# Performance work log

Measured on AMD Instinct MI355X. Metric: run time of the kernel, lower is better.

## Reference

```python
import jax, jax.numpy as jnp
import numpy as np

COMMITMENT_COST = 0.25


def setup_inputs() -> dict:
    key = jax.random.key(0)
    k1, k2 = jax.random.split(key)
    B, C, L, H, W = 4, 64, 16, 32, 32
    K = 1024
    inputs = jax.random.normal(k1, (B, C, L, H, W), dtype=jnp.float32)
    # matches torch init: uniform_(-1/K, 1/K)
    codebook = jax.random.uniform(k2, (K, C), dtype=jnp.float32,
                                  minval=-1.0 / K, maxval=1.0 / K)
    return {"inputs": inputs, "codebook": codebook}


def reference(inputs, codebook):
    B, C, L, H, W = inputs.shape
    # [B,C,L,H,W] -> [N, D] with D == embedding_dim == C
    x = jnp.transpose(inputs, (0, 2, 3, 4, 1)).reshape(-1, C).astype(jnp.float32)
    cb = codebook.astype(jnp.float32)
    # squared euclidean distances (argmin identical to p=2 cdist argmin)
    d2 = (jnp.sum(x * x, axis=1, keepdims=True)
          - 2.0 * (x @ cb.T)
          + jnp.sum(cb * cb, axis=1))  # [N, K]
    encoding_indices = jnp.argmin(d2, axis=1)  # [N]
    # one-hot @ codebook == direct gather
    quantized = cb[encoding_indices].astype(inputs.dtype)  # [N, D]
    quantized = jnp.transpose(quantized.reshape(B, L, H, W, C), (0, 4, 1, 2, 3))
    e_latent_loss = jnp.mean((jax.lax.stop_gradient(quantized) - inputs) ** 2)
    q_latent_loss = jnp.mean((quantized - jax.lax.stop_gradient(inputs)) ** 2)
    loss = q_latent_loss + COMMITMENT_COST * e_latent_loss
    # straight-through estimator
    quantized_st = inputs + jax.lax.stop_gradient(quantized - inputs)
    return quantized_st, loss, encoding_indices[:, None]
```

## Files before the change

kernel.cpp:

```cpp
#include <hip/hip_runtime.h>

constexpr int Cc   = 64;
constexpr int Kc   = 1024;
constexpr int Dc   = 64;
constexpr int LHWc = 16 * 32 * 32;
constexpr int Nc   = 4 * LHWc;
constexpr int QSIZE    = 4 * Cc * LHWc;
constexpr int OFF_LOSS = QSIZE;
constexpr int OFF_IDX  = QSIZE + 1;

constexpr int BLK_ROWS = 256;
constexpr int XPAD     = 68;

typedef __attribute__((ext_vector_type(8))) short short8;
typedef __attribute__((ext_vector_type(4))) float f32x4;

static __device__ __forceinline__ unsigned short f2bf(float f) {
    unsigned u = __float_as_uint(f);
    u += 0x7FFFu + ((u >> 16) & 1u);
    return (unsigned short)(u >> 16);
}
static __device__ __forceinline__ float bf2f(unsigned short h) {
    return __uint_as_float(((unsigned)h) << 16);
}

__global__ __launch_bounds__(256) void vq_prep(
    const float* __restrict__ cb, float* __restrict__ out,
    unsigned short* __restrict__ cbh, unsigned short* __restrict__ cbl,
    float* __restrict__ c2)
{
    const int t  = threadIdx.x;
    const int k0 = blockIdx.x * 64;
    if (blockIdx.x == 0 && t == 0) out[OFF_LOSS] = 0.0f;

    const int d  = t & 63;
#pragma unroll
    for (int r = 0; r < 16; ++r) {
        const int k = k0 + r * 4 + (t >> 6);
        const float v = cb[(size_t)k * Dc + d];
        unsigned short h = f2bf(v);
        cbh[(size_t)k * Dc + d] = h;
        cbl[(size_t)k * Dc + d] = f2bf(v - bf2f(h));
    }
    if (t < 64) {
        const int k = k0 + t;
        const float* c = cb + (size_t)k * Dc;
        float s = 0.f;
#pragma unroll
        for (int dd = 0; dd < Dc; ++dd) s = __builtin_fmaf(c[dd], c[dd], s);
        c2[k] = s;
    }
}

__global__ __launch_bounds__(512, 2) void vq_main(
    const float* __restrict__ in, const float* __restrict__ codebook,
    const unsigned short* __restrict__ cbh,
    const unsigned short* __restrict__ cbl,
    const float* __restrict__ c2g, float* __restrict__ out)
{
    __shared__ float  xs[BLK_ROWS][XPAD];
    __shared__ float  xs2[BLK_ROWS];
    __shared__ short8 xfh[2048];
    __shared__ short8 xfl[2048];
    __shared__ float  candV1[8][BLK_ROWS];
    __shared__ float  candV2[8][BLK_ROWS];
    __shared__ unsigned candKs[8][BLK_ROWS];
    __shared__ int    kws[BLK_ROWS];

    const int tid  = threadIdx.x;
    const int lane = tid & 63;
    const int w    = __builtin_amdgcn_readfirstlane(tid >> 6);
    const int col  = lane & 15;
    const int g    = lane >> 4;

    const int bq = blockIdx.x >> 6;
    const int p0 = (blockIdx.x & 63) * BLK_ROWS;
    const size_t inBase = (size_t)bq * (Cc * LHWc) + p0;

#pragma unroll
    for (int i = 0; i < 32; ++i) {
        int idx = i * 512 + tid;
        int d = idx >> 8, row = idx & 255;
        xs[row][d] = in[inBase + (size_t)d * LHWc + row];
    }
    __syncthreads();

    if (tid < BLK_ROWS) {
        float s = 0.f;
#pragma unroll
        for (int d = 0; d < Dc; ++d) s = __builtin_fmaf(xs[tid][d], xs[tid][d], s);
        xs2[tid] = s;
    }

#pragma unroll
    for (int j = 0; j < 4; ++j) {
        const int c  = tid + j * 512;
        const int t  = c >> 7;
        const int kt = (c >> 6) & 1;
        const int l  = c & 63;
        const int row = t * 16 + (l & 15);
        const int d0  = kt * 32 + (l >> 4) * 8;
        f32x4 v0 = *(const f32x4*)&xs[row][d0];
        f32x4 v1 = *(const f32x4*)&xs[row][d0 + 4];
        short8 h8, l8;
#pragma unroll
        for (int e = 0; e < 4; ++e) {
            unsigned short ha = f2bf(v0[e]);
            h8[e]     = (short)ha;
            l8[e]     = (short)f2bf(v0[e] - bf2f(ha));
            unsigned short hb = f2bf(v1[e]);
            h8[4 + e] = (short)hb;
            l8[4 + e] = (short)f2bf(v1[e] - bf2f(hb));
        }
        xfh[c] = h8; xfl[c] = l8;
    }
    __syncthreads();

    short8 Ah[8][2], Al[8][2];
    const size_t cbase = (size_t)(w * 128 + col) * Dc + g * 8;
#pragma unroll
    for (int ct = 0; ct < 8; ++ct) {
#pragma unroll
        for (int kt = 0; kt < 2; ++kt) {
            Ah[ct][kt] = *(const short8*)(cbh + cbase + ct * 16 * Dc + kt * 32);
            Al[ct][kt] = *(const short8*)(cbl + cbase + ct * 16 * Dc + kt * 32);
        }
    }
    float c2r[8][4];
#pragma unroll
    for (int ct = 0; ct < 8; ++ct)
#pragma unroll
        for (int r = 0; r < 4; ++r)
            c2r[ct][r] = c2g[w * 128 + ct * 16 + g * 4 + r];
    const int kbl = w * 128 + g * 4;

#pragma unroll 1
    for (int t = 0; t < 16; ++t) {
        const short8 xh0 = xfh[t * 128 + lane];
        const short8 xh1 = xfh[t * 128 + 64 + lane];
        const short8 xl0 = xfl[t * 128 + lane];
        const short8 xl1 = xfl[t * 128 + 64 + lane];
        const float  x2l = xs2[t * 16 + col];

        float bV = 3.4e38f, sV = 3.4e38f;
        int   bK = 0, sK = 0;

#pragma unroll
        for (int ct = 0; ct < 8; ++ct) {
            f32x4 acc = {0.f, 0.f, 0.f, 0.f};
            acc = __builtin_amdgcn_mfma_f32_16x16x32_bf16(Ah[ct][0], xh0, acc, 0, 0, 0);
            acc = __builtin_amdgcn_mfma_f32_16x16x32_bf16(Ah[ct][1], xh1, acc, 0, 0, 0);
            acc = __builtin_amdgcn_mfma_f32_16x16x32_bf16(Ah[ct][0], xl0, acc, 0, 0, 0);
            acc = __builtin_amdgcn_mfma_f32_16x16x32_bf16(Ah[ct][1], xl1, acc, 0, 0, 0);
            acc = __builtin_amdgcn_mfma_f32_16x16x32_bf16(Al[ct][0], xh0, acc, 0, 0, 0);
            acc = __builtin_amdgcn_mfma_f32_16x16x32_bf16(Al[ct][1], xh1, acc, 0, 0, 0);
#pragma unroll
            for (int r = 0; r < 4; ++r) {
                float d2 = __builtin_fmaf(-2.f, acc[r], x2l);
                float v  = d2 + c2r[ct][r];
                int   k  = kbl + ct * 16 + r;
                bool  c1 = v < bV;
                float nb  = c1 ? v : bV;
                int   nbk = c1 ? k : bK;
                float mx  = c1 ? bV : v;
                int   mxk = c1 ? bK : k;
                bool  c2_ = mx < sV;
                sV = c2_ ? mx : sV;
                sK = c2_ ? mxk : sK;
                bV = nb; bK = nbk;
            }
        }

#pragma unroll
        for (int m = 16; m <= 32; m <<= 1) {
            float ob  = __shfl_xor(bV, m, 64);
            int   obk = __shfl_xor(bK, m, 64);
            float os  = __shfl_xor(sV, m, 64);
            int   osk = __shfl_xor(sK, m, 64);
            bool  c1 = ob < bV;
            float nb  = c1 ? ob : bV;
            int   nbk = c1 ? obk : bK;
            float mx  = c1 ? bV : ob;
            int   mxk = c1 ? bK : obk;
            bool  c3 = os < sV;
            float ms  = c3 ? os : sV;
            int   msk = c3 ? osk : sK;
            bool  c4 = mx < ms;
            sV = c4 ? mx : ms;
            sK = c4 ? mxk : msk;
            bV = nb; bK = nbk;
        }
        if (g == 0) {
            const int row = t * 16 + col;
            candV1[w][row] = bV;
            candV2[w][row] = sV;
            candKs[w][row] = (unsigned)bK | ((unsigned)sK << 16);
        }
    }
    __syncthreads();

    if (tid < BLK_ROWS) {
        const int row = tid;
        unsigned long long b = ~0ull, s = ~0ull;
#pragma unroll
        for (int wv = 0; wv < 8; ++wv) {
            unsigned ks = candKs[wv][row];
            unsigned long long p1 =
                ((unsigned long long)__float_as_uint(candV1[wv][row]) << 32) | (ks & 0xFFFFu);
            unsigned long long p2 =
                ((unsigned long long)__float_as_uint(candV2[wv][row]) << 32) | (ks >> 16);
            unsigned long long nb = p1 < b ? p1 : b;
            unsigned long long mx = p1 < b ? b : p1;
            s = mx < s ? mx : s; b = nb;
            nb = p2 < b ? p2 : b;
            mx = p2 < b ? b : p2;
            s = mx < s ? mx : s; b = nb;
        }
        kws[row] = (int)((b & 0x3FFu) | ((s & 0x3FFu) << 16));
    }
    __syncthreads();

    {
        const int row = tid >> 1;
        const int ci  = tid & 1;
        const int pr  = kws[row];
        const int k   = ci ? ((pr >> 16) & 0x3FF) : (pr & 0x3FF);
        const float* cbr = codebook + (size_t)k * Dc;
        float a0 = 0.f, a1 = 0.f, a2 = 0.f, a3 = 0.f;
#pragma unroll
        for (int d16 = 0; d16 < 4; ++d16) {
            f32x4 cv0 = *(const f32x4*)(cbr + d16 * 16);
            f32x4 cv1 = *(const f32x4*)(cbr + d16 * 16 + 4);
            f32x4 cv2 = *(const f32x4*)(cbr + d16 * 16 + 8);
            f32x4 cv3 = *(const f32x4*)(cbr + d16 * 16 + 12);
            const float* xr = &xs[row][d16 * 16];
#pragma unroll
            for (int e = 0; e < 4; ++e) {
                a0 = __builtin_fmaf(xr[e],      cv0[e], a0);
                a1 = __builtin_fmaf(xr[4 + e],  cv1[e], a1);
                a2 = __builtin_fmaf(xr[8 + e],  cv2[e], a2);
                a3 = __builtin_fmaf(xr[12 + e], cv3[e], a3);
            }
        }
        float a  = (a0 + a1) + (a2 + a3);
        float d2 = __builtin_fmaf(-2.f, a, xs2[row]) + c2g[k];
        unsigned long long pk =
            ((unsigned long long)__float_as_uint(d2) << 32) | (unsigned)k;
        unsigned long long o = __shfl_xor(pk, 1, 64);
        pk = o < pk ? o : pk;
        if (ci == 0) {
            const int kwin = (int)(pk & 0x3FFu);
            kws[row] = kwin;
            out[OFF_IDX + (size_t)blockIdx.x * BLK_ROWS + row] = (float)kwin;
        }
    }
    __syncthreads();

    {
        const int row = tid & 255;
        const int cp  = tid >> 8;
        const int kw  = kws[row];
        const float* cbw = codebook + (size_t)kw * Dc + cp * 32;
        float* qout = out + inBase + row;
        float ls = 0.f;
#pragma unroll
        for (int j = 0; j < 32; ++j) {
            const int c = cp * 32 + j;
            float qv = cbw[j];
            qout[(size_t)c * LHWc] = qv;
            float e = qv - xs[row][c];
            ls = __builtin_fmaf(e, e, ls);
        }
#pragma unroll
        for (int off = 32; off > 0; off >>= 1) ls += __shfl_down(ls, off, 64);
        if (lane == 0) atomicAdd(&out[OFF_LOSS], ls * (1.25f / (float)QSIZE));
    }
}

extern "C" void kernel_launch(void* const* d_in, const int* in_sizes, int n_in,
                              void* d_out, int out_size, void* d_ws, size_t ws_size,
                              hipStream_t stream) {
    const float* in = (const float*)d_in[0];
    const float* cb = (const float*)d_in[1];
    float* out = (float*)d_out;
    (void)in_sizes; (void)n_in; (void)out_size; (void)ws_size;

    unsigned short* cbh = (unsigned short*)d_ws;
    unsigned short* cbl = cbh + (size_t)Kc * Dc;
    float*          c2  = (float*)(cbl + (size_t)Kc * Dc);

    vq_prep<<<dim3(16), dim3(256), 0, stream>>>(cb, out, cbh, cbl, c2);
    vq_main<<<dim3(Nc / BLK_ROWS), dim3(512), 0, stream>>>(in, cb, cbh, cbl, c2, out);
}
```

Baseline: 139.3 us.

## Restructure VQ kernel to 128-row blocks with 16 waves and no fp32 smem tile

Halves rows per block and doubles waves to 16 per 1024-thread block, so each wave holds 64 codebook entries in registers instead of 128. The fp32 input tile in shared memory is dropped: inputs are read from global memory straight into the bf16 hi/lo fragments, with partial squared norms computed on the fly. The per-row x² term is left out of the argmin scan, and a +0.25 offset is folded into c2. The exact rescoring and loss stages re-read inputs from global memory, and the candidate merge is split across two threads per row. The aim is lower register and LDS pressure and better occupancy, at the cost of extra global re-reads of the inputs.

```diff
diff --git a/kernel.cpp b/kernel.cpp
--- a/kernel.cpp
+++ b/kernel.cpp
@@ -9,8 +9,8 @@
 constexpr int OFF_LOSS = QSIZE;
 constexpr int OFF_IDX  = QSIZE + 1;
 
-constexpr int BLK_ROWS = 256;
-constexpr int XPAD     = 68;
+constexpr int BLK_ROWS = 128;
+constexpr int WAVES    = 16;
 
 typedef __attribute__((ext_vector_type(8))) short short8;
 typedef __attribute__((ext_vector_type(4))) float f32x4;
@@ -52,20 +52,20 @@
     }
 }
 
-__global__ __launch_bounds__(512, 2) void vq_main(
+__global__ __launch_bounds__(1024) void vq_main(
     const float* __restrict__ in, const float* __restrict__ codebook,
     const unsigned short* __restrict__ cbh,
     const unsigned short* __restrict__ cbl,
     const float* __restrict__ c2g, float* __restrict__ out)
 {
-    __shared__ float  xs[BLK_ROWS][XPAD];
-    __shared__ float  xs2[BLK_ROWS];
-    __shared__ short8 xfh[2048];
-    __shared__ short8 xfl[2048];
-    __shared__ float  candV1[8][BLK_ROWS];
-    __shared__ float  candV2[8][BLK_ROWS];
-    __shared__ unsigned candKs[8][BLK_ROWS];
-    __shared__ int    kws[BLK_ROWS];
+    __shared__ short8   xfh[1024];
+    __shared__ short8   xfl[1024];
+    __shared__ float    xpart[BLK_ROWS][8];
+    __shared__ float    xs2[BLK_ROWS];
+    __shared__ float    cV1[WAVES][BLK_ROWS];
+    __shared__ float    cV2[WAVES][BLK_ROWS];
+    __shared__ unsigned cK [WAVES][BLK_ROWS];
+    __shared__ unsigned kpack[BLK_ROWS];
 
     const int tid  = threadIdx.x;
     const int lane = tid & 63;
@@ -73,80 +73,67 @@
     const int col  = lane & 15;
     const int g    = lane >> 4;
 
-    const int bq = blockIdx.x >> 6;
-    const int p0 = (blockIdx.x & 63) * BLK_ROWS;
+    const int bq = blockIdx.x >> 7;
+    const int p0 = (blockIdx.x & 127) * BLK_ROWS;
     const size_t inBase = (size_t)bq * (Cc * LHWc) + p0;
 
-#pragma unroll
-    for (int i = 0; i < 32; ++i) {
-        int idx = i * 512 + tid;
-        int d = idx >> 8, row = idx & 255;
-        xs[row][d] = in[inBase + (size_t)d * LHWc + row];
-    }
-    __syncthreads();
-
-    if (tid < BLK_ROWS) {
-        float s = 0.f;
-#pragma unroll
-        for (int d = 0; d < Dc; ++d) s = __builtin_fmaf(xs[tid][d], xs[tid][d], s);
-        xs2[tid] = s;
-    }
-
-#pragma unroll
-    for (int j = 0; j < 4; ++j) {
-        const int c  = tid + j * 512;
+    short8 Ah[4][2], Al[4][2];
+    float  c2r[4][4];
+#pragma unroll
+    for (int ct = 0; ct < 4; ++ct) {
+        const size_t cb0 = (size_t)(w * 64 + ct * 16 + col) * Dc + g * 8;
+#pragma unroll
+        for (int kt = 0; kt < 2; ++kt) {
+            Ah[ct][kt] = *(const short8*)(cbh + cb0 + kt * 32);
+            Al[ct][kt] = *(const short8*)(cbl + cb0 + kt * 32);
+        }
+#pragma unroll
+        for (int r = 0; r < 4; ++r)
+            c2r[ct][r] = c2g[w * 64 + ct * 16 + g * 4 + r] + 0.25f;
+    }
+
+    {
+        const int c  = tid;
         const int t  = c >> 7;
         const int kt = (c >> 6) & 1;
-        const int l  = c & 63;
-        const int row = t * 16 + (l & 15);
-        const int d0  = kt * 32 + (l >> 4) * 8;
-        f32x4 v0 = *(const f32x4*)&xs[row][d0];
-        f32x4 v1 = *(const f32x4*)&xs[row][d0 + 4];
+        const int gi = (c >> 4) & 3;
+        const int cl = c & 15;
+        const int row = t * 16 + cl;
+        const float* xp = in + inBase + (size_t)(kt * 32 + gi * 8) * LHWc + row;
+        float v[8];
+#pragma unroll
+        for (int j = 0; j < 8; ++j) v[j] = xp[(size_t)j * LHWc];
+        float p = 0.f;
+#pragma unroll
+        for (int j = 0; j < 8; ++j) p = __builtin_fmaf(v[j], v[j], p);
         short8 h8, l8;
 #pragma unroll
-        for (int e = 0; e < 4; ++e) {
-            unsigned short ha = f2bf(v0[e]);
-            h8[e]     = (short)ha;
-            l8[e]     = (short)f2bf(v0[e] - bf2f(ha));
-            unsigned short hb = f2bf(v1[e]);
-            h8[4 + e] = (short)hb;
-            l8[4 + e] = (short)f2bf(v1[e] - bf2f(hb));
+        for (int j = 0; j < 8; ++j) {
+            unsigned short hv = f2bf(v[j]);
+            h8[j] = (short)hv;
+            l8[j] = (short)f2bf(v[j] - bf2f(hv));
         }
         xfh[c] = h8; xfl[c] = l8;
-    }
-    __syncthreads();
-
-    short8 Ah[8][2], Al[8][2];
-    const size_t cbase = (size_t)(w * 128 + col) * Dc + g * 8;
-#pragma unroll
-    for (int ct = 0; ct < 8; ++ct) {
-#pragma unroll
-        for (int kt = 0; kt < 2; ++kt) {
-            Ah[ct][kt] = *(const short8*)(cbh + cbase + ct * 16 * Dc + kt * 32);
-            Al[ct][kt] = *(const short8*)(cbl + cbase + ct * 16 * Dc + kt * 32);
-        }
-    }
-    float c2r[8][4];
-#pragma unroll
-    for (int ct = 0; ct < 8; ++ct)
-#pragma unroll
-        for (int r = 0; r < 4; ++r)
-            c2r[ct][r] = c2g[w * 128 + ct * 16 + g * 4 + r];
-    const int kbl = w * 128 + g * 4;
+        xpart[row][kt * 4 + gi] = p;
+    }
+    __syncthreads();
+    if (tid < BLK_ROWS) {
+        const float* q = xpart[tid];
+        xs2[tid] = ((q[0] + q[1]) + (q[2] + q[3])) + ((q[4] + q[5]) + (q[6] + q[7]));
+    }
 
 #pragma unroll 1
-    for (int t = 0; t < 16; ++t) {
+    for (int t = 0; t < 8; ++t) {
         const short8 xh0 = xfh[t * 128 + lane];
         const short8 xh1 = xfh[t * 128 + 64 + lane];
         const short8 xl0 = xfl[t * 128 + lane];
         const short8 xl1 = xfl[t * 128 + 64 + lane];
-        const float  x2l = xs2[t * 16 + col];
 
         float bV = 3.4e38f, sV = 3.4e38f;
         int   bK = 0, sK = 0;
 
 #pragma unroll
-        for (int ct = 0; ct < 8; ++ct) {
+        for (int ct = 0; ct < 4; ++ct) {
             f32x4 acc = {0.f, 0.f, 0.f, 0.f};
             acc = __builtin_amdgcn_mfma_f32_16x16x32_bf16(Ah[ct][0], xh0, acc, 0, 0, 0);
             acc = __builtin_amdgcn_mfma_f32_16x16x32_bf16(Ah[ct][1], xh1, acc, 0, 0, 0);
@@ -156,13 +143,12 @@
             acc = __builtin_amdgcn_mfma_f32_16x16x32_bf16(Al[ct][1], xh1, acc, 0, 0, 0);
 #pragma unroll
             for (int r = 0; r < 4; ++r) {
-                float d2 = __builtin_fmaf(-2.f, acc[r], x2l);
-                float v  = d2 + c2r[ct][r];
-                int   k  = kbl + ct * 16 + r;
-                bool  c1 = v < bV;
-                float nb  = c1 ? v : bV;
+                float vv = __builtin_fmaf(-2.f, acc[r], c2r[ct][r]);
+                const int k = w * 64 + ct * 16 + g * 4 + r;
+                bool  c1 = vv < bV;
+                float nb  = c1 ? vv : bV;
                 int   nbk = c1 ? k : bK;
-                float mx  = c1 ? bV : v;
+                float mx  = c1 ? bV : vv;
                 int   mxk = c1 ? bK : k;
                 bool  c2_ = mx < sV;
                 sV = c2_ ? mx : sV;
@@ -192,55 +178,73 @@
         }
         if (g == 0) {
             const int row = t * 16 + col;
-            candV1[w][row] = bV;
-            candV2[w][row] = sV;
-            candKs[w][row] = (unsigned)bK | ((unsigned)sK << 16);
-        }
-    }
-    __syncthreads();
-
-    if (tid < BLK_ROWS) {
-        const int row = tid;
-        unsigned long long b = ~0ull, s = ~0ull;
+            cV1[w][row] = bV;
+            cV2[w][row] = sV;
+            cK [w][row] = (unsigned)bK | ((unsigned)sK << 16);
+        }
+    }
+    __syncthreads();
+
+    if (tid < 2 * BLK_ROWS) {
+        const int row = tid >> 1;
+        const int h   = tid & 1;
+        float b = 3.4e38f, s = 3.4e38f;
+        int   bk = 0, sk = 0;
 #pragma unroll
         for (int wv = 0; wv < 8; ++wv) {
-            unsigned ks = candKs[wv][row];
-            unsigned long long p1 =
-                ((unsigned long long)__float_as_uint(candV1[wv][row]) << 32) | (ks & 0xFFFFu);
-            unsigned long long p2 =
-                ((unsigned long long)__float_as_uint(candV2[wv][row]) << 32) | (ks >> 16);
-            unsigned long long nb = p1 < b ? p1 : b;
-            unsigned long long mx = p1 < b ? b : p1;
-            s = mx < s ? mx : s; b = nb;
-            nb = p2 < b ? p2 : b;
-            mx = p2 < b ? b : p2;
-            s = mx < s ? mx : s; b = nb;
-        }
-        kws[row] = (int)((b & 0x3FFu) | ((s & 0x3FFu) << 16));
-    }
-    __syncthreads();
-
-    {
+            const int wj = h * 8 + wv;
+            const unsigned ks = cK[wj][row];
+            const float v1 = cV1[wj][row];
+            const float v2 = cV2[wj][row];
+            const int  k1 = (int)(ks & 0xFFFFu);
+            const int  k2 = (int)(ks >> 16);
+            {
+                bool c1 = v1 < b;
+                float mx = c1 ? b : v1;  int mxk = c1 ? bk : k1;
+                b  = c1 ? v1 : b;        bk  = c1 ? k1 : bk;
+                bool c2_ = mx < s;  s = c2_ ? mx : s;  sk = c2_ ? mxk : sk;
+            }
+            {
+                bool c1 = v2 < b;
+                float mx = c1 ? b : v2;  int mxk = c1 ? bk : k2;
+                b  = c1 ? v2 : b;        bk  = c1 ? k2 : bk;
+                bool c2_ = mx < s;  s = c2_ ? mx : s;  sk = c2_ ? mxk : sk;
+            }
+        }
+        float ob  = __shfl_xor(b, 1, 64);
+        int   obk = __shfl_xor(bk, 1, 64);
+        float os  = __shfl_xor(s, 1, 64);
+        int   osk = __shfl_xor(sk, 1, 64);
+        if (h == 0) {
+            bool  c1 = ob < b;
+            float nb  = c1 ? ob : b;
+            int   nbk = c1 ? obk : bk;
+            float mx  = c1 ? b : ob;
+            int   mxk = c1 ? bk : obk;
+            bool  c3 = os < s;
+            float ms  = c3 ? os : s;
+            int   msk = c3 ? osk : sk;
+            bool  c4 = mx < ms;
+            int   fsk = c4 ? mxk : msk;
+            kpack[row] = (unsigned)nbk | ((unsigned)fsk << 16);
+        }
+    }
+    __syncthreads();
+
+    if (tid < 2 * BLK_ROWS) {
         const int row = tid >> 1;
         const int ci  = tid & 1;
-        const int pr  = kws[row];
-        const int k   = ci ? ((pr >> 16) & 0x3FF) : (pr & 0x3FF);
+        const unsigned pr = kpack[row];
+        const int k = ci ? (int)(pr >> 16) : (int)(pr & 0xFFFFu);
         const float* cbr = codebook + (size_t)k * Dc;
+        const float* xr  = in + inBase + row;
         float a0 = 0.f, a1 = 0.f, a2 = 0.f, a3 = 0.f;
 #pragma unroll
-        for (int d16 = 0; d16 < 4; ++d16) {
-            f32x4 cv0 = *(const f32x4*)(cbr + d16 * 16);
-            f32x4 cv1 = *(const f32x4*)(cbr + d16 * 16 + 4);
-            f32x4 cv2 = *(const f32x4*)(cbr + d16 * 16 + 8);
-            f32x4 cv3 = *(const f32x4*)(cbr + d16 * 16 + 12);
-            const float* xr = &xs[row][d16 * 16];
-#pragma unroll
-            for (int e = 0; e < 4; ++e) {
-                a0 = __builtin_fmaf(xr[e],      cv0[e], a0);
-                a1 = __builtin_fmaf(xr[4 + e],  cv1[e], a1);
-                a2 = __builtin_fmaf(xr[8 + e],  cv2[e], a2);
-                a3 = __builtin_fmaf(xr[12 + e], cv3[e], a3);
-            }
+        for (int d = 0; d < 64; d += 4) {
+            a0 = __builtin_fmaf(xr[(size_t)(d + 0) * LHWc], cbr[d + 0], a0);
+            a1 = __builtin_fmaf(xr[(size_t)(d + 1) * LHWc], cbr[d + 1], a1);
+            a2 = __builtin_fmaf(xr[(size_t)(d + 2) * LHWc], cbr[d + 2], a2);
+            a3 = __builtin_fmaf(xr[(size_t)(d + 3) * LHWc], cbr[d + 3], a3);
         }
         float a  = (a0 + a1) + (a2 + a3);
         float d2 = __builtin_fmaf(-2.f, a, xs2[row]) + c2g[k];
@@ -250,25 +254,26 @@
         pk = o < pk ? o : pk;
         if (ci == 0) {
             const int kwin = (int)(pk & 0x3FFu);
-            kws[row] = kwin;
+            kpack[row] = (unsigned)kwin;
             out[OFF_IDX + (size_t)blockIdx.x * BLK_ROWS + row] = (float)kwin;
         }
     }
     __syncthreads();
 
     {
-        const int row = tid & 255;
-        const int cp  = tid >> 8;
-        const int kw  = kws[row];
-        const float* cbw = codebook + (size_t)kw * Dc + cp * 32;
+        const int row = tid & 127;
+        const int cp  = tid >> 7;
+        const int kw  = (int)kpack[row];
+        const float* cbw = codebook + (size_t)kw * Dc + cp * 8;
+        const float* xr  = in + inBase + row;
         float* qout = out + inBase + row;
         float ls = 0.f;
 #pragma unroll
-        for (int j = 0; j < 32; ++j) {
-            const int c = cp * 32 + j;
+        for (int j = 0; j < 8; ++j) {
+            const int c = cp * 8 + j;
             float qv = cbw[j];
             qout[(size_t)c * LHWc] = qv;
-            float e = qv - xs[row][c];
+            float e = qv - xr[(size_t)c * LHWc];
             ls = __builtin_fmaf(e, e, ls);
         }
 #pragma unroll
@@ -290,5 +295,5 @@
     float*          c2  = (float*)(cbl + (size_t)Kc * Dc);
 
     vq_prep<<<dim3(16), dim3(256), 0, stream>>>(cb, out, cbh, cbl, c2);
-    vq_main<<<dim3(Nc / BLK_ROWS), dim3(512), 0, stream>>>(in, cb, cbh, cbl, c2, out);
-}
+    vq_main<<<dim3(Nc / BLK_ROWS), dim3(1024), 0, stream>>>(in, cb, cbh, cbl, c2, out);
+}
```

Measured after the change: 202.6 us. 45.4% more time.

## Fold codebook prep into main kernel and seed MFMA accumulators with -c2/2

Applied to the files above, without the earlier changes.

Removes the separate prep kernel, so each block now computes codebook squared norms into shared memory and converts the codebook to bf16 hi/lo fragments in registers directly from fp32. The distance expression is rewritten as a max over dot minus half the norm, by seeding the MFMA accumulator with -0.5*c2. This drops the per-element x2 add and -2 scaling, and the top-2 tracking becomes a per-register fmax chain. The cross-wave candidate merge is split over all 512 threads, and the x tile padding changes to 65. The cost is that every block redundantly reads the full codebook and recomputes its norms, which adds global traffic and prologue work per block.

```diff
diff --git a/kernel.cpp b/kernel.cpp
--- a/kernel.cpp
+++ b/kernel.cpp
@@ -10,7 +10,8 @@
 constexpr int OFF_IDX  = QSIZE + 1;
 
 constexpr int BLK_ROWS = 256;
-constexpr int XPAD     = 68;
+constexpr int NW       = 8;
+constexpr int XPAD     = 65;
 
 typedef __attribute__((ext_vector_type(8))) short short8;
 typedef __attribute__((ext_vector_type(4))) float f32x4;
@@ -24,48 +25,24 @@
     return __uint_as_float(((unsigned)h) << 16);
 }
 
-__global__ __launch_bounds__(256) void vq_prep(
-    const float* __restrict__ cb, float* __restrict__ out,
-    unsigned short* __restrict__ cbh, unsigned short* __restrict__ cbl,
-    float* __restrict__ c2)
+__global__ void vq_zero(float* __restrict__ out) {
+    out[OFF_LOSS] = 0.0f;
+}
+
+__global__ __launch_bounds__(512)
+__attribute__((amdgpu_waves_per_eu(2, 2))) void vq_main(
+    const float* __restrict__ in, const float* __restrict__ codebook,
+    float* __restrict__ out)
 {
-    const int t  = threadIdx.x;
-    const int k0 = blockIdx.x * 64;
-    if (blockIdx.x == 0 && t == 0) out[OFF_LOSS] = 0.0f;
-
-    const int d  = t & 63;
-#pragma unroll
-    for (int r = 0; r < 16; ++r) {
-        const int k = k0 + r * 4 + (t >> 6);
-        const float v = cb[(size_t)k * Dc + d];
-        unsigned short h = f2bf(v);
-        cbh[(size_t)k * Dc + d] = h;
-        cbl[(size_t)k * Dc + d] = f2bf(v - bf2f(h));
-    }
-    if (t < 64) {
-        const int k = k0 + t;
-        const float* c = cb + (size_t)k * Dc;
-        float s = 0.f;
-#pragma unroll
-        for (int dd = 0; dd < Dc; ++dd) s = __builtin_fmaf(c[dd], c[dd], s);
-        c2[k] = s;
-    }
-}
-
-__global__ __launch_bounds__(512, 2) void vq_main(
-    const float* __restrict__ in, const float* __restrict__ codebook,
-    const unsigned short* __restrict__ cbh,
-    const unsigned short* __restrict__ cbl,
-    const float* __restrict__ c2g, float* __restrict__ out)
-{
-    __shared__ float  xs[BLK_ROWS][XPAD];
-    __shared__ float  xs2[BLK_ROWS];
-    __shared__ short8 xfh[2048];
-    __shared__ short8 xfl[2048];
-    __shared__ float  candV1[8][BLK_ROWS];
-    __shared__ float  candV2[8][BLK_ROWS];
-    __shared__ unsigned candKs[8][BLK_ROWS];
-    __shared__ int    kws[BLK_ROWS];
+    __shared__ float    xs[BLK_ROWS][XPAD];
+    __shared__ short8   xfh[2048];
+    __shared__ short8   xfl[2048];
+    __shared__ float    c2s[Kc];
+    __shared__ float    xs2[BLK_ROWS];
+    __shared__ float    cV1[NW][BLK_ROWS];
+    __shared__ float    cV2[NW][BLK_ROWS];
+    __shared__ unsigned cK [NW][BLK_ROWS];
+    __shared__ unsigned kws[BLK_ROWS];
 
     const int tid  = threadIdx.x;
     const int lane = tid & 63;
@@ -82,6 +59,38 @@
         int idx = i * 512 + tid;
         int d = idx >> 8, row = idx & 255;
         xs[row][d] = in[inBase + (size_t)d * LHWc + row];
+    }
+
+#pragma unroll
+    for (int j = 0; j < 2; ++j) {
+        const int k = tid + j * 512;
+        const float* c = codebook + (size_t)k * Dc;
+        float s = 0.f;
+#pragma unroll
+        for (int d = 0; d < Dc; ++d) s = __builtin_fmaf(c[d], c[d], s);
+        c2s[k] = s;
+    }
+
+    short8 Ah[8][2], Al[8][2];
+#pragma unroll
+    for (int ct = 0; ct < 8; ++ct) {
+        const float* cr = codebook + (size_t)(w * 128 + ct * 16 + col) * Dc + g * 8;
+#pragma unroll
+        for (int kt = 0; kt < 2; ++kt) {
+            f32x4 v0 = *(const f32x4*)(cr + kt * 32);
+            f32x4 v1 = *(const f32x4*)(cr + kt * 32 + 4);
+            short8 h8, l8;
+#pragma unroll
+            for (int e = 0; e < 4; ++e) {
+                unsigned short ha = f2bf(v0[e]);
+                h8[e]     = (short)ha;
+                l8[e]     = (short)f2bf(v0[e] - bf2f(ha));
+                unsigned short hb = f2bf(v1[e]);
+                h8[4 + e] = (short)hb;
+                l8[4 + e] = (short)f2bf(v1[e] - bf2f(hb));
+            }
+            Ah[ct][kt] = h8; Al[ct][kt] = l8;
+        }
     }
     __syncthreads();
 
@@ -114,25 +123,17 @@
         }
         xfh[c] = h8; xfl[c] = l8;
     }
-    __syncthreads();
-
-    short8 Ah[8][2], Al[8][2];
-    const size_t cbase = (size_t)(w * 128 + col) * Dc + g * 8;
+
+    f32x4 seed[8];
 #pragma unroll
     for (int ct = 0; ct < 8; ++ct) {
-#pragma unroll
-        for (int kt = 0; kt < 2; ++kt) {
-            Ah[ct][kt] = *(const short8*)(cbh + cbase + ct * 16 * Dc + kt * 32);
-            Al[ct][kt] = *(const short8*)(cbl + cbase + ct * 16 * Dc + kt * 32);
-        }
-    }
-    float c2r[8][4];
-#pragma unroll
-    for (int ct = 0; ct < 8; ++ct)
-#pragma unroll
-        for (int r = 0; r < 4; ++r)
-            c2r[ct][r] = c2g[w * 128 + ct * 16 + g * 4 + r];
-    const int kbl = w * 128 + g * 4;
+        f32x4 cv = *(const f32x4*)&c2s[w * 128 + ct * 16 + g * 4];
+#pragma unroll
+        for (int e = 0; e < 4; ++e) seed[ct][e] = -0.5f * (cv[e] + 0.25f);
+    }
+    __syncthreads();
+
+    const int kb = w * 128 + g * 4;
 
 #pragma unroll 1
     for (int t = 0; t < 16; ++t) {
@@ -140,14 +141,17 @@
         const short8 xh1 = xfh[t * 128 + 64 + lane];
         const short8 xl0 = xfl[t * 128 + lane];
         const short8 xl1 = xfl[t * 128 + 64 + lane];
-        const float  x2l = xs2[t * 16 + col];
-
-        float bV = 3.4e38f, sV = 3.4e38f;
-        int   bK = 0, sK = 0;
+
+        float bV[4], sV[4];
+        int   bK[4], sK[4];
+#pragma unroll
+        for (int r = 0; r < 4; ++r) {
+            bV[r] = -3.4e38f; sV[r] = -3.4e38f; bK[r] = 0; sK[r] = 0;
+        }
 
 #pragma unroll
         for (int ct = 0; ct < 8; ++ct) {
-            f32x4 acc = {0.f, 0.f, 0.f, 0.f};
+            f32x4 acc = seed[ct];
             acc = __builtin_amdgcn_mfma_f32_16x16x32_bf16(Ah[ct][0], xh0, acc, 0, 0, 0);
             acc = __builtin_amdgcn_mfma_f32_16x16x32_bf16(Ah[ct][1], xh1, acc, 0, 0, 0);
             acc = __builtin_amdgcn_mfma_f32_16x16x32_bf16(Ah[ct][0], xl0, acc, 0, 0, 0);
@@ -156,84 +160,124 @@
             acc = __builtin_amdgcn_mfma_f32_16x16x32_bf16(Al[ct][1], xh1, acc, 0, 0, 0);
 #pragma unroll
             for (int r = 0; r < 4; ++r) {
-                float d2 = __builtin_fmaf(-2.f, acc[r], x2l);
-                float v  = d2 + c2r[ct][r];
-                int   k  = kbl + ct * 16 + r;
-                bool  c1 = v < bV;
-                float nb  = c1 ? v : bV;
-                int   nbk = c1 ? k : bK;
-                float mx  = c1 ? bV : v;
-                int   mxk = c1 ? bK : k;
-                bool  c2_ = mx < sV;
-                sV = c2_ ? mx : sV;
-                sK = c2_ ? mxk : sK;
-                bV = nb; bK = nbk;
-            }
+                const float a  = acc[r];
+                const int   k  = kb + ct * 16 + r;
+                const float mn = fminf(a, bV[r]);
+                const bool  c1 = a > bV[r];
+                const int  mnk = c1 ? bK[r] : k;
+                bV[r] = fmaxf(a, bV[r]);
+                bK[r] = c1 ? k : bK[r];
+                const bool c2_ = mn > sV[r];
+                sV[r] = fmaxf(mn, sV[r]);
+                sK[r] = c2_ ? mnk : sK[r];
+            }
+        }
+
+        float b = bV[0], s = sV[0];
+        int   bk = bK[0], sk = sK[0];
+#pragma unroll
+        for (int r = 1; r < 4; ++r) {
+            const bool  c1 = bV[r] > b;
+            const float nb  = c1 ? bV[r] : b;
+            const int   nbk = c1 ? bK[r] : bk;
+            const float mn  = c1 ? b : bV[r];
+            const int   mnk = c1 ? bk : bK[r];
+            const float so  = c1 ? sV[r] : s;
+            const int   sok = c1 ? sK[r] : sk;
+            const bool  c2_ = so > mn;
+            s  = c2_ ? so : mn;
+            sk = c2_ ? sok : mnk;
+            b = nb; bk = nbk;
         }
 
 #pragma unroll
         for (int m = 16; m <= 32; m <<= 1) {
-            float ob  = __shfl_xor(bV, m, 64);
-            int   obk = __shfl_xor(bK, m, 64);
-            float os  = __shfl_xor(sV, m, 64);
-            int   osk = __shfl_xor(sK, m, 64);
-            bool  c1 = ob < bV;
-            float nb  = c1 ? ob : bV;
-            int   nbk = c1 ? obk : bK;
-            float mx  = c1 ? bV : ob;
-            int   mxk = c1 ? bK : obk;
-            bool  c3 = os < sV;
-            float ms  = c3 ? os : sV;
-            int   msk = c3 ? osk : sK;
-            bool  c4 = mx < ms;
-            sV = c4 ? mx : ms;
-            sK = c4 ? mxk : msk;
-            bV = nb; bK = nbk;
+            const float ob  = __shfl_xor(b, m, 64);
+            const int   obk = __shfl_xor(bk, m, 64);
+            const float os  = __shfl_xor(s, m, 64);
+            const int   osk = __shfl_xor(sk, m, 64);
+            const bool  c1 = ob > b;
+            const float nb  = c1 ? ob : b;
+            const int   nbk = c1 ? obk : bk;
+            const float mn  = c1 ? b : ob;
+            const int   mnk = c1 ? bk : obk;
+            const bool  c3 = os > s;
+            const float ms  = c3 ? os : s;
+            const int   msk = c3 ? osk : sk;
+            const bool  c4 = mn > ms;
+            s  = c4 ? mn : ms;
+            sk = c4 ? mnk : msk;
+            b = nb; bk = nbk;
         }
         if (g == 0) {
             const int row = t * 16 + col;
-            candV1[w][row] = bV;
-            candV2[w][row] = sV;
-            candKs[w][row] = (unsigned)bK | ((unsigned)sK << 16);
-        }
-    }
-    __syncthreads();
-
-    if (tid < BLK_ROWS) {
-        const int row = tid;
-        unsigned long long b = ~0ull, s = ~0ull;
-#pragma unroll
-        for (int wv = 0; wv < 8; ++wv) {
-            unsigned ks = candKs[wv][row];
-            unsigned long long p1 =
-                ((unsigned long long)__float_as_uint(candV1[wv][row]) << 32) | (ks & 0xFFFFu);
-            unsigned long long p2 =
-                ((unsigned long long)__float_as_uint(candV2[wv][row]) << 32) | (ks >> 16);
-            unsigned long long nb = p1 < b ? p1 : b;
-            unsigned long long mx = p1 < b ? b : p1;
-            s = mx < s ? mx : s; b = nb;
-            nb = p2 < b ? p2 : b;
-            mx = p2 < b ? b : p2;
-            s = mx < s ? mx : s; b = nb;
-        }
-        kws[row] = (int)((b & 0x3FFu) | ((s & 0x3FFu) << 16));
+            cV1[w][row] = b;
+            cV2[w][row] = s;
+            cK [w][row] = (unsigned)bk | ((unsigned)sk << 16);
+        }
+    }
+    __syncthreads();
+
+    {
+        const int row = tid >> 1;
+        const int h   = tid & 1;
+        float b = -3.4e38f, s = -3.4e38f;
+        int   bk = 0, sk = 0;
+#pragma unroll
+        for (int wv = 0; wv < 4; ++wv) {
+            const int wj = h * 4 + wv;
+            const unsigned ks = cK[wj][row];
+            const float v1 = cV1[wj][row];
+            const float v2 = cV2[wj][row];
+            const int  k1 = (int)(ks & 0xFFFFu);
+            const int  k2 = (int)(ks >> 16);
+            {
+                const bool c1 = v1 > b;
+                const float mn = c1 ? b : v1;  const int mnk = c1 ? bk : k1;
+                b  = c1 ? v1 : b;              bk  = c1 ? k1 : bk;
+                const bool c2_ = mn > s;  s = c2_ ? mn : s;  sk = c2_ ? mnk : sk;
+            }
+            {
+                const bool c1 = v2 > b;
+                const float mn = c1 ? b : v2;  const int mnk = c1 ? bk : k2;
+                b  = c1 ? v2 : b;              bk  = c1 ? k2 : bk;
+                const bool c2_ = mn > s;  s = c2_ ? mn : s;  sk = c2_ ? mnk : sk;
+            }
+        }
+        const float ob  = __shfl_xor(b, 1, 64);
+        const int   obk = __shfl_xor(bk, 1, 64);
+        const float os  = __shfl_xor(s, 1, 64);
+        const int   osk = __shfl_xor(sk, 1, 64);
+        if (h == 0) {
+            const bool  c1 = ob > b;
+            const float nb  = c1 ? ob : b;
+            const int   nbk = c1 ? obk : bk;
+            const float mn  = c1 ? b : ob;
+            const int   mnk = c1 ? bk : obk;
+            const bool  c3 = os > s;
+            const float ms  = c3 ? os : s;
+            const int   msk = c3 ? osk : sk;
+            const bool  c4 = mn > ms;
+            const int   fsk = c4 ? mnk : msk;
+            kws[row] = (unsigned)nbk | ((unsigned)fsk << 16);
+        }
     }
     __syncthreads();
 
     {
         const int row = tid >> 1;
         const int ci  = tid & 1;
-        const int pr  = kws[row];
-        const int k   = ci ? ((pr >> 16) & 0x3FF) : (pr & 0x3FF);
+        const unsigned pr = kws[row];
+        const int k = ci ? (int)(pr >> 16) : (int)(pr & 0xFFFFu);
         const float* cbr = codebook + (size_t)k * Dc;
         float a0 = 0.f, a1 = 0.f, a2 = 0.f, a3 = 0.f;
 #pragma unroll
-        for (int d16 = 0; d16 < 4; ++d16) {
-            f32x4 cv0 = *(const f32x4*)(cbr + d16 * 16);
-            f32x4 cv1 = *(const f32x4*)(cbr + d16 * 16 + 4);
-            f32x4 cv2 = *(const f32x4*)(cbr + d16 * 16 + 8);
-            f32x4 cv3 = *(const f32x4*)(cbr + d16 * 16 + 12);
-            const float* xr = &xs[row][d16 * 16];
+        for (int d4 = 0; d4 < 4; ++d4) {
+            f32x4 cv0 = *(const f32x4*)(cbr + d4 * 16);
+            f32x4 cv1 = *(const f32x4*)(cbr + d4 * 16 + 4);
+            f32x4 cv2 = *(const f32x4*)(cbr + d4 * 16 + 8);
+            f32x4 cv3 = *(const f32x4*)(cbr + d4 * 16 + 12);
+            const float* xr = &xs[row][d4 * 16];
 #pragma unroll
             for (int e = 0; e < 4; ++e) {
                 a0 = __builtin_fmaf(xr[e],      cv0[e], a0);
@@ -242,15 +286,15 @@
                 a3 = __builtin_fmaf(xr[12 + e], cv3[e], a3);
             }
         }
-        float a  = (a0 + a1) + (a2 + a3);
-        float d2 = __builtin_fmaf(-2.f, a, xs2[row]) + c2g[k];
+        const float a  = (a0 + a1) + (a2 + a3);
+        const float d2 = __builtin_fmaf(-2.f, a, xs2[row]) + c2s[k];
         unsigned long long pk =
             ((unsigned long long)__float_as_uint(d2) << 32) | (unsigned)k;
-        unsigned long long o = __shfl_xor(pk, 1, 64);
+        const unsigned long long o = __shfl_xor(pk, 1, 64);
         pk = o < pk ? o : pk;
         if (ci == 0) {
             const int kwin = (int)(pk & 0x3FFu);
-            kws[row] = kwin;
+            kws[row] = (unsigned)kwin;
             out[OFF_IDX + (size_t)blockIdx.x * BLK_ROWS + row] = (float)kwin;
         }
     }
@@ -259,7 +303,7 @@
     {
         const int row = tid & 255;
         const int cp  = tid >> 8;
-        const int kw  = kws[row];
+        const int kw  = (int)kws[row];
         const float* cbw = codebook + (size_t)kw * Dc + cp * 32;
         float* qout = out + inBase + row;
         float ls = 0.f;
@@ -283,12 +327,8 @@
     const float* in = (const float*)d_in[0];
     const float* cb = (const float*)d_in[1];
     float* out = (float*)d_out;
-    (void)in_sizes; (void)n_in; (void)out_size; (void)ws_size;
-
-    unsigned short* cbh = (unsigned short*)d_ws;
-    unsigned short* cbl = cbh + (size_t)Kc * Dc;
-    float*          c2  = (float*)(cbl + (size_t)Kc * Dc);
-
-    vq_prep<<<dim3(16), dim3(256), 0, stream>>>(cb, out, cbh, cbl, c2);
-    vq_main<<<dim3(Nc / BLK_ROWS), dim3(512), 0, stream>>>(in, cb, cbh, cbl, c2, out);
-}
+    (void)in_sizes; (void)n_in; (void)out_size; (void)d_ws; (void)ws_size;
+
+    vq_zero<<<dim3(1), dim3(1), 0, stream>>>(out);
+    vq_main<<<dim3(Nc / BLK_ROWS), dim3(512), 0, stream>>>(in, cb, out);
+}
```

Measured after the change: 164.9 us. 1.18x slower.

## Fold codebook norms into MFMA accumulator init and rescore all wave candidates exactly

Applied to the files above, without the earlier changes.

The argmin becomes an argmax of x·c − 0.5·|c|², because |x|² is constant per row. The precomputed −0.5·|c|² is loaded from shared memory as the initial MFMA accumulator, which removes the per-element FMA/add and the 32 registers that held codebook norms in the hot loop. The cross-wave top-2 merge by approximate values is dropped. Instead each row's 16 candidate indices (top-2 from each of 8 waves) are rescored in exact fp32, split across two threads. This adds codebook gathers and a 64-float register array in the refinement phase in exchange for less VALU work in the main loop.

```diff
diff --git a/kernel.cpp b/kernel.cpp
--- a/kernel.cpp
+++ b/kernel.cpp
@@ -10,6 +10,7 @@
 constexpr int OFF_IDX  = QSIZE + 1;
 
 constexpr int BLK_ROWS = 256;
+constexpr int NW       = 8;
 constexpr int XPAD     = 68;
 
 typedef __attribute__((ext_vector_type(8))) short short8;
@@ -27,7 +28,7 @@
 __global__ __launch_bounds__(256) void vq_prep(
     const float* __restrict__ cb, float* __restrict__ out,
     unsigned short* __restrict__ cbh, unsigned short* __restrict__ cbl,
-    float* __restrict__ c2)
+    float* __restrict__ c2, float* __restrict__ c2n)
 {
     const int t  = threadIdx.x;
     const int k0 = blockIdx.x * 64;
@@ -48,7 +49,8 @@
         float s = 0.f;
 #pragma unroll
         for (int dd = 0; dd < Dc; ++dd) s = __builtin_fmaf(c[dd], c[dd], s);
-        c2[k] = s;
+        c2[k]  = s;
+        c2n[k] = -0.5f * (s + 0.25f);
     }
 }
 
@@ -56,16 +58,16 @@
     const float* __restrict__ in, const float* __restrict__ codebook,
     const unsigned short* __restrict__ cbh,
     const unsigned short* __restrict__ cbl,
-    const float* __restrict__ c2g, float* __restrict__ out)
+    const float* __restrict__ c2g, const float* __restrict__ c2ng,
+    float* __restrict__ out)
 {
-    __shared__ float  xs[BLK_ROWS][XPAD];
-    __shared__ float  xs2[BLK_ROWS];
-    __shared__ short8 xfh[2048];
-    __shared__ short8 xfl[2048];
-    __shared__ float  candV1[8][BLK_ROWS];
-    __shared__ float  candV2[8][BLK_ROWS];
-    __shared__ unsigned candKs[8][BLK_ROWS];
-    __shared__ int    kws[BLK_ROWS];
+    __shared__ float    xs[BLK_ROWS][XPAD];
+    __shared__ short8   xfh[2048];
+    __shared__ short8   xfl[2048];
+    __shared__ float    c2ns[Kc];
+    __shared__ float    xs2[BLK_ROWS];
+    __shared__ unsigned cK[NW][BLK_ROWS];
+    __shared__ unsigned kws[BLK_ROWS];
 
     const int tid  = threadIdx.x;
     const int lane = tid & 63;
@@ -77,6 +79,8 @@
     const int p0 = (blockIdx.x & 63) * BLK_ROWS;
     const size_t inBase = (size_t)bq * (Cc * LHWc) + p0;
 
+    c2ns[tid]       = c2ng[tid];
+    c2ns[tid + 512] = c2ng[tid + 512];
 #pragma unroll
     for (int i = 0; i < 32; ++i) {
         int idx = i * 512 + tid;
@@ -114,25 +118,20 @@
         }
         xfh[c] = h8; xfl[c] = l8;
     }
-    __syncthreads();
 
     short8 Ah[8][2], Al[8][2];
-    const size_t cbase = (size_t)(w * 128 + col) * Dc + g * 8;
 #pragma unroll
     for (int ct = 0; ct < 8; ++ct) {
+        const size_t cb0 = (size_t)(w * 128 + ct * 16 + col) * Dc + g * 8;
 #pragma unroll
         for (int kt = 0; kt < 2; ++kt) {
-            Ah[ct][kt] = *(const short8*)(cbh + cbase + ct * 16 * Dc + kt * 32);
-            Al[ct][kt] = *(const short8*)(cbl + cbase + ct * 16 * Dc + kt * 32);
-        }
-    }
-    float c2r[8][4];
-#pragma unroll
-    for (int ct = 0; ct < 8; ++ct)
-#pragma unroll
-        for (int r = 0; r < 4; ++r)
-            c2r[ct][r] = c2g[w * 128 + ct * 16 + g * 4 + r];
-    const int kbl = w * 128 + g * 4;
+            Ah[ct][kt] = *(const short8*)(cbh + cb0 + kt * 32);
+            Al[ct][kt] = *(const short8*)(cbl + cb0 + kt * 32);
+        }
+    }
+    __syncthreads();
+
+    const int kb = w * 128 + g * 4;
 
 #pragma unroll 1
     for (int t = 0; t < 16; ++t) {
@@ -140,14 +139,13 @@
         const short8 xh1 = xfh[t * 128 + 64 + lane];
         const short8 xl0 = xfl[t * 128 + lane];
         const short8 xl1 = xfl[t * 128 + 64 + lane];
-        const float  x2l = xs2[t * 16 + col];
-
-        float bV = 3.4e38f, sV = 3.4e38f;
+
+        float bV = -3.4e38f, sV = -3.4e38f;
         int   bK = 0, sK = 0;
 
 #pragma unroll
         for (int ct = 0; ct < 8; ++ct) {
-            f32x4 acc = {0.f, 0.f, 0.f, 0.f};
+            f32x4 acc = *(const f32x4*)&c2ns[w * 128 + ct * 16 + g * 4];
             acc = __builtin_amdgcn_mfma_f32_16x16x32_bf16(Ah[ct][0], xh0, acc, 0, 0, 0);
             acc = __builtin_amdgcn_mfma_f32_16x16x32_bf16(Ah[ct][1], xh1, acc, 0, 0, 0);
             acc = __builtin_amdgcn_mfma_f32_16x16x32_bf16(Ah[ct][0], xl0, acc, 0, 0, 0);
@@ -156,101 +154,85 @@
             acc = __builtin_amdgcn_mfma_f32_16x16x32_bf16(Al[ct][1], xh1, acc, 0, 0, 0);
 #pragma unroll
             for (int r = 0; r < 4; ++r) {
-                float d2 = __builtin_fmaf(-2.f, acc[r], x2l);
-                float v  = d2 + c2r[ct][r];
-                int   k  = kbl + ct * 16 + r;
-                bool  c1 = v < bV;
-                float nb  = c1 ? v : bV;
-                int   nbk = c1 ? k : bK;
-                float mx  = c1 ? bV : v;
-                int   mxk = c1 ? bK : k;
-                bool  c2_ = mx < sV;
-                sV = c2_ ? mx : sV;
-                sK = c2_ ? mxk : sK;
+                const float a = acc[r];
+                const int   k = kb + ct * 16 + r;
+                const bool  c1 = a > bV;
+                const float nb  = c1 ? a : bV;
+                const int   nbk = c1 ? k : bK;
+                const float mn  = c1 ? bV : a;
+                const int   mnk = c1 ? bK : k;
+                const bool  c2_ = mn > sV;
+                sV = c2_ ? mn : sV;
+                sK = c2_ ? mnk : sK;
                 bV = nb; bK = nbk;
             }
         }
 
 #pragma unroll
         for (int m = 16; m <= 32; m <<= 1) {
-            float ob  = __shfl_xor(bV, m, 64);
-            int   obk = __shfl_xor(bK, m, 64);
-            float os  = __shfl_xor(sV, m, 64);
-            int   osk = __shfl_xor(sK, m, 64);
-            bool  c1 = ob < bV;
-            float nb  = c1 ? ob : bV;
-            int   nbk = c1 ? obk : bK;
-            float mx  = c1 ? bV : ob;
-            int   mxk = c1 ? bK : obk;
-            bool  c3 = os < sV;
-            float ms  = c3 ? os : sV;
-            int   msk = c3 ? osk : sK;
-            bool  c4 = mx < ms;
-            sV = c4 ? mx : ms;
-            sK = c4 ? mxk : msk;
+            const float ob  = __shfl_xor(bV, m, 64);
+            const int   obk = __shfl_xor(bK, m, 64);
+            const float os  = __shfl_xor(sV, m, 64);
+            const int   osk = __shfl_xor(sK, m, 64);
+            const bool  c1 = ob > bV;
+            const float nb  = c1 ? ob : bV;
+            const int   nbk = c1 ? obk : bK;
+            const float mn  = c1 ? bV : ob;
+            const int   mnk = c1 ? bK : obk;
+            const bool  c3 = os > sV;
+            const float ms  = c3 ? os : sV;
+            const int   msk = c3 ? osk : sK;
+            const bool  c4 = mn > ms;
+            sV = c4 ? mn : ms;
+            sK = c4 ? mnk : msk;
             bV = nb; bK = nbk;
         }
         if (g == 0) {
-            const int row = t * 16 + col;
-            candV1[w][row] = bV;
-            candV2[w][row] = sV;
-            candKs[w][row] = (unsigned)bK | ((unsigned)sK << 16);
-        }
-    }
-    __syncthreads();
-
-    if (tid < BLK_ROWS) {
-        const int row = tid;
-        unsigned long long b = ~0ull, s = ~0ull;
-#pragma unroll
-        for (int wv = 0; wv < 8; ++wv) {
-            unsigned ks = candKs[wv][row];
-            unsigned long long p1 =
-                ((unsigned long long)__float_as_uint(candV1[wv][row]) << 32) | (ks & 0xFFFFu);
-            unsigned long long p2 =
-                ((unsigned long long)__float_as_uint(candV2[wv][row]) << 32) | (ks >> 16);
-            unsigned long long nb = p1 < b ? p1 : b;
-            unsigned long long mx = p1 < b ? b : p1;
-            s = mx < s ? mx : s; b = nb;
-            nb = p2 < b ? p2 : b;
-            mx = p2 < b ? b : p2;
-            s = mx < s ? mx : s; b = nb;
-        }
-        kws[row] = (int)((b & 0x3FFu) | ((s & 0x3FFu) << 16));
+            cK[w][t * 16 + col] = (unsigned)bK | ((unsigned)sK << 16);
+        }
     }
     __syncthreads();
 
     {
         const int row = tid >> 1;
-        const int ci  = tid & 1;
-        const int pr  = kws[row];
-        const int k   = ci ? ((pr >> 16) & 0x3FF) : (pr & 0x3FF);
-        const float* cbr = codebook + (size_t)k * Dc;
-        float a0 = 0.f, a1 = 0.f, a2 = 0.f, a3 = 0.f;
-#pragma unroll
-        for (int d16 = 0; d16 < 4; ++d16) {
-            f32x4 cv0 = *(const f32x4*)(cbr + d16 * 16);
-            f32x4 cv1 = *(const f32x4*)(cbr + d16 * 16 + 4);
-            f32x4 cv2 = *(const f32x4*)(cbr + d16 * 16 + 8);
-            f32x4 cv3 = *(const f32x4*)(cbr + d16 * 16 + 12);
-            const float* xr = &xs[row][d16 * 16];
-#pragma unroll
-            for (int e = 0; e < 4; ++e) {
-                a0 = __builtin_fmaf(xr[e],      cv0[e], a0);
-                a1 = __builtin_fmaf(xr[4 + e],  cv1[e], a1);
-                a2 = __builtin_fmaf(xr[8 + e],  cv2[e], a2);
-                a3 = __builtin_fmaf(xr[12 + e], cv3[e], a3);
+        const int h   = tid & 1;
+        float x[64];
+#pragma unroll
+        for (int d4 = 0; d4 < 16; ++d4) {
+            f32x4 xv = *(const f32x4*)&xs[row][d4 * 4];
+            x[d4 * 4 + 0] = xv[0]; x[d4 * 4 + 1] = xv[1];
+            x[d4 * 4 + 2] = xv[2]; x[d4 * 4 + 3] = xv[3];
+        }
+        const float x2 = xs2[row];
+
+        unsigned long long best = ~0ull;
+#pragma unroll
+        for (int wv = 0; wv < 4; ++wv) {
+            const unsigned ks = cK[h * 4 + wv][row];
+#pragma unroll
+            for (int ci = 0; ci < 2; ++ci) {
+                const int k = ci ? (int)(ks >> 16) : (int)(ks & 0xFFFFu);
+                const float* cbr = codebook + (size_t)k * Dc;
+                float a0 = 0.f, a1 = 0.f, a2 = 0.f, a3 = 0.f;
+#pragma unroll
+                for (int d = 0; d < 64; d += 4) {
+                    a0 = __builtin_fmaf(x[d + 0], cbr[d + 0], a0);
+                    a1 = __builtin_fmaf(x[d + 1], cbr[d + 1], a1);
+                    a2 = __builtin_fmaf(x[d + 2], cbr[d + 2], a2);
+                    a3 = __builtin_fmaf(x[d + 3], cbr[d + 3], a3);
+                }
+                const float a  = (a0 + a1) + (a2 + a3);
+                const float d2 = __builtin_fmaf(-2.f, a, x2) + c2g[k];
+                unsigned long long pk =
+                    ((unsigned long long)__float_as_uint(d2) << 32) | (unsigned)k;
+                best = pk < best ? pk : best;
             }
         }
-        float a  = (a0 + a1) + (a2 + a3);
-        float d2 = __builtin_fmaf(-2.f, a, xs2[row]) + c2g[k];
-        unsigned long long pk =
-            ((unsigned long long)__float_as_uint(d2) << 32) | (unsigned)k;
-        unsigned long long o = __shfl_xor(pk, 1, 64);
-        pk = o < pk ? o : pk;
-        if (ci == 0) {
-            const int kwin = (int)(pk & 0x3FFu);
-            kws[row] = kwin;
+        const unsigned long long o = __shfl_xor(best, 1, 64);
+        best = o < best ? o : best;
+        if (h == 0) {
+            const int kwin = (int)(best & 0x3FFu);
+            kws[row] = (unsigned)kwin;
             out[OFF_IDX + (size_t)blockIdx.x * BLK_ROWS + row] = (float)kwin;
         }
     }
@@ -259,7 +241,7 @@
     {
         const int row = tid & 255;
         const int cp  = tid >> 8;
-        const int kw  = kws[row];
+        const int kw  = (int)kws[row];
         const float* cbw = codebook + (size_t)kw * Dc + cp * 32;
         float* qout = out + inBase + row;
         float ls = 0.f;
@@ -288,7 +270,8 @@
     unsigned short* cbh = (unsigned short*)d_ws;
     unsigned short* cbl = cbh + (size_t)Kc * Dc;
     float*          c2  = (float*)(cbl + (size_t)Kc * Dc);
-
-    vq_prep<<<dim3(16), dim3(256), 0, stream>>>(cb, out, cbh, cbl, c2);
-    vq_main<<<dim3(Nc / BLK_ROWS), dim3(512), 0, stream>>>(in, cb, cbh, cbl, c2, out);
-}
+    float*          c2n = c2 + Kc;
+
+    vq_prep<<<dim3(16), dim3(256), 0, stream>>>(cb, out, cbh, cbl, c2, c2n);
+    vq_main<<<dim3(Nc / BLK_ROWS), dim3(512), 0, stream>>>(in, cb, cbh, cbl, c2, c2n, out);
+}
```

New measurement: 162.9 us. 1.17x slower.
